# Kernel tuning notes

Measured on AMD Instinct MI355X. Metric: run time of the kernel, lower is better.

## Reference

```python
import jax, jax.numpy as jnp
import numpy as np

NUM_HEADS = 16
CHUNK = 64
RMS_EPS = 1.1920928955078125e-07  # torch.finfo(float32).eps, F.rms_norm default


def setup_inputs() -> dict:
    key = jax.random.key(0)
    k1, k2, k3 = jax.random.split(key, 3)
    B, S, D = 2, 4096, 2048
    x = jax.random.normal(k1, (B, S, D), dtype=jnp.float32)
    w_in = jax.random.normal(k2, (5 * D, D), dtype=jnp.float32) * 0.02
    w_out = jax.random.normal(k3, (D, D), dtype=jnp.float32) * 0.02
    return {"x": x, "w_in": w_in, "w_out": w_out}


def _forward(x, w_in, w_out):
    B, S, D = x.shape
    H, hd, C = NUM_HEADS, D // NUM_HEADS, CHUNK
    proj = x @ w_in.T                              # [B,S,5D]
    q, k, v, a, g = jnp.split(proj, 5, axis=-1)
    rs = lambda t: t.reshape(B, S, H, hd)
    q, k, v, a, g = map(rs, (q, k, v, a, g))
    # rms_norm over head_dim, no learned weight
    q = q * jax.lax.rsqrt(jnp.mean(q * q, axis=-1, keepdims=True) + RMS_EPS)
    k = jnp.tanh(k)
    a = jnp.clip(jax.nn.sigmoid(a + 2.0), 0.6, 0.9995)
    u = k * v                                      # updates, float32
    NC = S // C
    # [NC, B, C, H, hd] so lax.scan iterates over chunks
    a_r = a.reshape(B, NC, C, H, hd).transpose(1, 0, 2, 3, 4)
    u_r = u.reshape(B, NC, C, H, hd).transpose(1, 0, 2, 3, 4)

    def step(state, au):
        a_c, u_c = au                              # [B,C,H,hd]
        prefix = jnp.cumprod(a_c, axis=1)
        acc = jnp.cumsum(u_c / jnp.maximum(prefix, 1e-6), axis=1)
        states = prefix * (state[:, None] + acc)   # [B,C,H,hd]
        return states[:, -1], states

    state0 = jnp.zeros((B, H, hd), dtype=jnp.float32)
    _, mem = jax.lax.scan(step, state0, (a_r, u_r))  # [NC,B,C,H,hd]
    memory = mem.transpose(1, 0, 2, 3, 4).reshape(B, S, H, hd)
    gate = jax.nn.sigmoid(g)
    y = gate * (q * memory) + (1.0 - gate) * v
    return y.reshape(B, S, D) @ w_out.T


def reference(x, w_in, w_out):
    return _forward(x, w_in, w_out)
```

## Files before the change

### kernel.cpp

```cpp
#include <hip/hip_runtime.h>
#include <cstdint>
#include <cstddef>

typedef unsigned short u16;
typedef __bf16 bf16x8 __attribute__((ext_vector_type(8)));
typedef unsigned int u32;
typedef u32 u32x4 __attribute__((ext_vector_type(4)));
typedef float f32x4v __attribute__((ext_vector_type(4)));

#define BB 2
#define SS 4096
#define DD 2048
#define HH 16
#define HD 128
#define CC 64
#define NC 64
#define D5 10240
#define RMS_EPS 1.1920928955078125e-07f

__device__ __forceinline__ u16 f2bf(float f) {
  uint32_t x = __float_as_uint(f);
  uint32_t r = (x + 0x7fffu + ((x >> 16) & 1u)) >> 16;
  return (u16)r;
}
__device__ __forceinline__ float bf2f(u16 u) {
  return __uint_as_float(((uint32_t)u) << 16);
}
__device__ __forceinline__ float fast_sigmoid(float x) {
  return 1.0f / (1.0f + __expf(-x));
}
__device__ __forceinline__ float fast_tanh(float x) {
  return 1.0f - 2.0f / (__expf(2.0f * x) + 1.0f);
}

__global__ void cvt_bf16x8_kernel(const f32x4v* __restrict__ src,
                                  u32x4* __restrict__ dst, int n8) {
  int i = blockIdx.x * blockDim.x + threadIdx.x;
  int stride = gridDim.x * blockDim.x;
  for (; i < n8; i += stride) {
    f32x4v a = src[2 * i];
    f32x4v b = src[2 * i + 1];
    u32x4 o;
    o.x = (u32)f2bf(a.x) | ((u32)f2bf(a.y) << 16);
    o.y = (u32)f2bf(a.z) | ((u32)f2bf(a.w) << 16);
    o.z = (u32)f2bf(b.x) | ((u32)f2bf(b.y) << 16);
    o.w = (u32)f2bf(b.z) | ((u32)f2bf(b.w) << 16);
    dst[i] = o;
  }
}

template <typename OutT>
__global__ __launch_bounds__(512, 2) void gemm_bt(const u16* __restrict__ A,
                                                  const u16* __restrict__ B,
                                                  OutT* __restrict__ C,
                                                  int M, int N, int K) {
  __shared__ u16 lds[65536];

  const int tid = threadIdx.x;
  const int wave = tid >> 6;
  const int lane = tid & 63;

  const int nwg = (int)gridDim.x;
  const int bid = (int)blockIdx.x;
  const int bswz = (bid & 7) * (nwg >> 3) + (bid >> 3);
  const int Mt = M >> 8;
  const int m0 = (bswz % Mt) << 8;
  const int n0 = (bswz / Mt) << 8;

  const int wm = (wave >> 2) << 7;
  const int wn = (wave & 3) << 6;

  const int s_r = tid >> 3;
  const int s_ls = (tid & 7) ^ (s_r & 7);
  const u16* Ast = A + (size_t)(m0 + s_r) * K + s_ls * 8;
  const u16* Bst = B + (size_t)(n0 + s_r) * K + s_ls * 8;
  const int s_lb = wave * 512;

  const int fr = lane & 15;
  const int fg = lane >> 4;
  const int fx = lane & 7;
  const int psk0 = ((0 + fg) ^ fx) * 8;
  const int psk1 = ((4 + fg) ^ fx) * 8;
  const int aro = (wm + fr) * 64;
  const int bro = 16384 + (wn + fr) * 64;

  f32x4v acc[8][4] = {};
  bf16x8 afr[4][2];
  bf16x8 bfr[2][2][2];
  const int NT = K >> 6;

#define BARF()                              \
  do {                                      \
    asm volatile("" ::: "memory");          \
    __builtin_amdgcn_s_barrier();           \
    asm volatile("" ::: "memory");          \
  } while (0)

#define STAGE(GB, LB, H, KT)                                                    \
  do {                                                                          \
    const u16* g_ = (GB) + (size_t)((H) * 128) * K + (KT) * 64;                 \
    __builtin_amdgcn_global_load_lds(                                           \
        (__attribute__((address_space(1))) void*)(u16*)g_,                      \
        (__attribute__((address_space(3))) void*)&lds[(LB) + (H) * 8192 + s_lb],\
        16, 0, 0);                                                              \
    __builtin_amdgcn_global_load_lds(                                           \
        (__attribute__((address_space(1))) void*)(u16*)(g_ + (size_t)64 * K),   \
        (__attribute__((address_space(3))) void*)&lds[(LB) + (H) * 8192 + 4096 + s_lb], \
        16, 0, 0);                                                              \
  } while (0)

#define LOADA(BO, MH)                                             \
  do {                                                            \
    _Pragma("unroll") for (int mf = 0; mf < 4; ++mf) {            \
      const int ab_ = (BO) + aro + (MH) * 4096 + mf * 1024;       \
      afr[mf][0] = *(const bf16x8*)&lds[ab_ + psk0];              \
      afr[mf][1] = *(const bf16x8*)&lds[ab_ + psk1];              \
    }                                                             \
  } while (0)

#define LOADB(BO, NH)                                             \
  do {                                                            \
    _Pragma("unroll") for (int nf = 0; nf < 2; ++nf) {            \
      const int bb_ = (BO) + bro + (NH) * 2048 + nf * 1024;       \
      bfr[NH][nf][0] = *(const bf16x8*)&lds[bb_ + psk0];          \
      bfr[NH][nf][1] = *(const bf16x8*)&lds[bb_ + psk1];          \
    }                                                             \
  } while (0)

#define MMAQ(MH, NH)                                                          \
  do {                                                                        \
    __builtin_amdgcn_s_setprio(1);                                            \
    _Pragma("unroll") for (int mf = 0; mf < 4; ++mf)                          \
        _Pragma("unroll") for (int nf = 0; nf < 2; ++nf) {                    \
      acc[(MH) * 4 + mf][(NH) * 2 + nf] =                                     \
          __builtin_amdgcn_mfma_f32_16x16x32_bf16(                            \
              afr[mf][0], bfr[NH][nf][0], acc[(MH) * 4 + mf][(NH) * 2 + nf],  \
              0, 0, 0);                                                       \
      acc[(MH) * 4 + mf][(NH) * 2 + nf] =                                     \
          __builtin_amdgcn_mfma_f32_16x16x32_bf16(                            \
              afr[mf][1], bfr[NH][nf][1], acc[(MH) * 4 + mf][(NH) * 2 + nf],  \
              0, 0, 0);                                                       \
    }                                                                         \
    __builtin_amdgcn_s_setprio(0);                                            \
    __builtin_amdgcn_sched_barrier(0);                                        \
  } while (0)

  STAGE(Ast, 0, 0, 0);
  STAGE(Ast, 0, 1, 0);
  STAGE(Bst, 16384, 0, 0);
  STAGE(Bst, 16384, 1, 0);
  {
    const int k1 = (NT > 1) ? 1 : 0;
    STAGE(Ast, 32768, 0, k1);
    STAGE(Ast, 32768, 1, k1);
    STAGE(Bst, 49152, 0, k1);
    STAGE(Bst, 49152, 1, k1);
  }
  asm volatile("s_waitcnt vmcnt(8)" ::: "memory");
  BARF();

  for (int t = 0; t < NT; ++t) {
    const int bo = (t & 1) << 15;
    const int t2 = (t + 2 < NT) ? t + 2 : NT - 1;

    LOADA(bo, 0);
    LOADB(bo, 0);
    BARF();
    MMAQ(0, 0);
    BARF();

    LOADB(bo, 1);
    BARF();
    MMAQ(0, 1);
    BARF();

    LOADA(bo, 1);
    BARF();
    MMAQ(1, 1);
    BARF();

    STAGE(Ast, bo, 0, t2);
    STAGE(Bst, bo + 16384, 0, t2);
    STAGE(Ast, bo, 1, t2);
    STAGE(Bst, bo + 16384, 1, t2);
    BARF();
    MMAQ(1, 0);
    asm volatile("s_waitcnt vmcnt(8)" ::: "memory");
    BARF();
  }

  asm volatile("s_waitcnt vmcnt(0)" ::: "memory");

  const int ccol = lane & 15;
  const int crow = (lane >> 4) << 2;
#pragma unroll
  for (int am = 0; am < 8; ++am) {
    const size_t r0 = (size_t)(m0 + wm + ((am >> 2) << 6) + ((am & 3) << 4) + crow);
#pragma unroll
    for (int an = 0; an < 4; ++an) {
      const size_t c0 = (size_t)(n0 + wn + ((an >> 1) << 5) + ((an & 1) << 4) + ccol);
#pragma unroll
      for (int r = 0; r < 4; ++r) {
        OutT* Cp = C + (r0 + r) * (size_t)N + c0;
        if constexpr (sizeof(OutT) == 2)
          *Cp = (OutT)f2bf(acc[am][an][r]);
        else
          *Cp = acc[am][an][r];
      }
    }
  }
#undef BARF
#undef STAGE
#undef LOADA
#undef LOADB
#undef MMAQ
}

__global__ __launch_bounds__(64) void scan_chunk(const u16* __restrict__ proj,
                                                 float* __restrict__ Pc,
                                                 float* __restrict__ Lc) {
  const int idx = blockIdx.x;
  const int h = idx & (HH - 1);
  const int c = (idx >> 4) & (NC - 1);
  const int b = idx >> 10;
  const int lane = threadIdx.x;

  const size_t row0 = (size_t)(b * SS + c * CC) * D5 + h * HD;

  float p0 = 1.0f, a0 = 0.0f, p1 = 1.0f, a1 = 0.0f;
  for (int t = 0; t < CC; ++t) {
    const size_t rp = row0 + (size_t)t * D5;
    float k0 = bf2f(proj[rp + DD + lane]);
    float k1 = bf2f(proj[rp + DD + lane + 64]);
    float v0 = bf2f(proj[rp + 2 * DD + lane]);
    float v1 = bf2f(proj[rp + 2 * DD + lane + 64]);
    float ar0 = bf2f(proj[rp + 3 * DD + lane]);
    float ar1 = bf2f(proj[rp + 3 * DD + lane + 64]);
    float aa0 = fminf(fmaxf(fast_sigmoid(ar0 + 2.0f), 0.6f), 0.9995f);
    float aa1 = fminf(fmaxf(fast_sigmoid(ar1 + 2.0f), 0.6f), 0.9995f);
    p0 *= aa0;
    p1 *= aa1;
    a0 += fast_tanh(k0) * v0 / fmaxf(p0, 1e-6f);
    a1 += fast_tanh(k1) * v1 / fmaxf(p1, 1e-6f);
  }
  const size_t ci = ((size_t)(b * NC + c) * HH + h) * HD;
  Pc[ci + lane] = p0;
  Pc[ci + lane + 64] = p1;
  Lc[ci + lane] = p0 * a0;
  Lc[ci + lane + 64] = p1 * a1;
}

__global__ void scan_carry(const float* __restrict__ Pc, const float* __restrict__ Lc,
                           float* __restrict__ Sin) {
  const int t = blockIdx.x * blockDim.x + threadIdx.x;
  const int b = t >> 11;
  const int hd = t & (DD - 1);
  float state = 0.0f;
  for (int c = 0; c < NC; ++c) {
    const size_t i = (size_t)(b * NC + c) * DD + hd;
    Sin[i] = state;
    state = Pc[i] * state + Lc[i];
  }
}

__global__ __launch_bounds__(64) void finalize_y(const u16* __restrict__ proj,
                                                 const float* __restrict__ Sin,
                                                 u16* __restrict__ y) {
  const int idx = blockIdx.x;
  const int h = idx & (HH - 1);
  const int c = (idx >> 4) & (NC - 1);
  const int b = idx >> 10;
  const int lane = threadIdx.x;

  const size_t row0 = (size_t)(b * SS + c * CC) * D5 + h * HD;
  const size_t out0 = (size_t)(b * SS + c * CC) * DD + h * HD;
  const size_t sinb = (size_t)(b * NC + c) * DD + h * HD;
  const float sin0 = Sin[sinb + lane];
  const float sin1 = Sin[sinb + lane + 64];

  float p0 = 1.0f, a0 = 0.0f, p1 = 1.0f, a1 = 0.0f;
  for (int t = 0; t < CC; ++t) {
    const size_t rp = row0 + (size_t)t * D5;
    const float q0 = bf2f(proj[rp + lane]);
    const float q1 = bf2f(proj[rp + lane + 64]);
    const float k0 = bf2f(proj[rp + DD + lane]);
    const float k1 = bf2f(proj[rp + DD + lane + 64]);
    const float v0 = bf2f(proj[rp + 2 * DD + lane]);
    const float v1 = bf2f(proj[rp + 2 * DD + lane + 64]);
    const float ar0 = bf2f(proj[rp + 3 * DD + lane]);
    const float ar1 = bf2f(proj[rp + 3 * DD + lane + 64]);
    const float g0 = bf2f(proj[rp + 4 * DD + lane]);
    const float g1 = bf2f(proj[rp + 4 * DD + lane + 64]);

    const float aa0 = fminf(fmaxf(fast_sigmoid(ar0 + 2.0f), 0.6f), 0.9995f);
    const float aa1 = fminf(fmaxf(fast_sigmoid(ar1 + 2.0f), 0.6f), 0.9995f);
    p0 *= aa0;
    p1 *= aa1;
    a0 += fast_tanh(k0) * v0 / fmaxf(p0, 1e-6f);
    a1 += fast_tanh(k1) * v1 / fmaxf(p1, 1e-6f);
    const float mem0 = p0 * (sin0 + a0);
    const float mem1 = p1 * (sin1 + a1);

    float ss = q0 * q0 + q1 * q1;
#pragma unroll
    for (int m = 32; m; m >>= 1) ss += __shfl_xor(ss, m);
    const float rn = rsqrtf(ss * (1.0f / 128.0f) + RMS_EPS);

    const float gt0 = fast_sigmoid(g0);
    const float gt1 = fast_sigmoid(g1);
    y[out0 + (size_t)t * DD + lane] = f2bf(gt0 * (q0 * rn * mem0) + (1.0f - gt0) * v0);
    y[out0 + (size_t)t * DD + lane + 64] = f2bf(gt1 * (q1 * rn * mem1) + (1.0f - gt1) * v1);
  }
}

extern "C" void kernel_launch(void* const* d_in, const int* in_sizes, int n_in,
                              void* d_out, int out_size, void* d_ws, size_t ws_size,
                              hipStream_t stream) {
  const float* x = (const float*)d_in[0];
  const float* w_in = (const float*)d_in[1];
  const float* w_out = (const float*)d_in[2];
  float* out = (float*)d_out;

  char* ws = (char*)d_ws;
  size_t off = 0;
  auto alloc = [&](size_t bytes) -> void* {
    void* p = ws + off;
    off += (bytes + 255) & ~(size_t)255;
    return p;
  };
  const size_t nBS = (size_t)BB * SS;
  u16* projb = (u16*)alloc(nBS * D5 * 2);
  u16* xb    = (u16*)alloc(nBS * DD * 2);
  u16* wib   = (u16*)alloc((size_t)D5 * DD * 2);
  u16* wob   = (u16*)alloc((size_t)DD * DD * 2);
  float* Pc  = (float*)alloc((size_t)BB * NC * DD * 4);
  float* Lc  = (float*)alloc((size_t)BB * NC * DD * 4);
  float* Sin = (float*)alloc((size_t)BB * NC * DD * 4);
  u16* yb = xb;
  (void)in_sizes; (void)n_in; (void)out_size;

  if (off > ws_size) return;

  cvt_bf16x8_kernel<<<1024, 256, 0, stream>>>((const f32x4v*)x, (u32x4*)xb,
                                              (int)(nBS * DD / 8));
  cvt_bf16x8_kernel<<<1024, 256, 0, stream>>>((const f32x4v*)w_in, (u32x4*)wib,
                                              (int)((size_t)D5 * DD / 8));
  cvt_bf16x8_kernel<<<1024, 256, 0, stream>>>((const f32x4v*)w_out, (u32x4*)wob,
                                              (int)((size_t)DD * DD / 8));

  gemm_bt<u16><<<dim3(32 * 40), 512, 0, stream>>>(xb, wib, projb, 8192, 10240, 2048);

  scan_chunk<<<BB * NC * HH, 64, 0, stream>>>(projb, Pc, Lc);

  scan_carry<<<16, 256, 0, stream>>>(Pc, Lc, Sin);

  finalize_y<<<BB * NC * HH, 64, 0, stream>>>(projb, Sin, yb);

  gemm_bt<float><<<dim3(32 * 8), 512, 0, stream>>>(yb, wob, out, 8192, 2048, 2048);
}
```

Before: 690.7 us.

## Remove intra-iteration barriers in GEMM loop and stage bf16 epilogue through LDS

Drops most workgroup barriers and sched_barriers inside the GEMM main loop. LDS fragment loads are now issued ahead of the MFMA groups so the compiler can interleave them, cutting sync stalls per k-tile. For bf16 output, the epilogue writes accumulators into a swizzled per-wave LDS tile and then stores 16-byte vectors to global memory, replacing scattered 2-byte stores. Fewer barriers risk correctness if the LDS staging buffer is overwritten while other waves still read it, and prefetching more fragments raises register pressure.

```diff
diff --git a/kernel.cpp b/kernel.cpp
--- a/kernel.cpp
+++ b/kernel.cpp
@@ -142,7 +142,6 @@
               0, 0, 0);                                                       \
     }                                                                         \
     __builtin_amdgcn_s_setprio(0);                                            \
-    __builtin_amdgcn_sched_barrier(0);                                        \
   } while (0)
 
   STAGE(Ast, 0, 0, 0);
@@ -165,47 +164,63 @@
 
     LOADA(bo, 0);
     LOADB(bo, 0);
-    BARF();
+    LOADB(bo, 1);
     MMAQ(0, 0);
-    BARF();
-
-    LOADB(bo, 1);
-    BARF();
     MMAQ(0, 1);
-    BARF();
-
     LOADA(bo, 1);
-    BARF();
     MMAQ(1, 1);
+    __builtin_amdgcn_sched_barrier(0);
     BARF();
 
     STAGE(Ast, bo, 0, t2);
     STAGE(Bst, bo + 16384, 0, t2);
     STAGE(Ast, bo, 1, t2);
     STAGE(Bst, bo + 16384, 1, t2);
-    BARF();
     MMAQ(1, 0);
     asm volatile("s_waitcnt vmcnt(8)" ::: "memory");
     BARF();
   }
 
   asm volatile("s_waitcnt vmcnt(0)" ::: "memory");
+  BARF();
 
   const int ccol = lane & 15;
   const int crow = (lane >> 4) << 2;
-#pragma unroll
-  for (int am = 0; am < 8; ++am) {
-    const size_t r0 = (size_t)(m0 + wm + ((am >> 2) << 6) + ((am & 3) << 4) + crow);
-#pragma unroll
-    for (int an = 0; an < 4; ++an) {
-      const size_t c0 = (size_t)(n0 + wn + ((an >> 1) << 5) + ((an & 1) << 4) + ccol);
-#pragma unroll
-      for (int r = 0; r < 4; ++r) {
-        OutT* Cp = C + (r0 + r) * (size_t)N + c0;
-        if constexpr (sizeof(OutT) == 2)
-          *Cp = (OutT)f2bf(acc[am][an][r]);
-        else
+  if constexpr (sizeof(OutT) == 2) {
+    u16* wlds = &lds[wave * 8192];
+#pragma unroll
+    for (int am = 0; am < 8; ++am) {
+#pragma unroll
+      for (int an = 0; an < 4; ++an) {
+        const int col = ((an >> 1) << 5) + ((an & 1) << 4) + ccol;
+        const int cch = col >> 3, cre = col & 7;
+#pragma unroll
+        for (int r = 0; r < 4; ++r) {
+          const int row = ((am >> 2) << 6) + ((am & 3) << 4) + crow + r;
+          wlds[row * 64 + ((cch ^ (row & 7)) << 3) + cre] =
+              f2bf(acc[am][an][r]);
+        }
+      }
+    }
+#pragma unroll
+    for (int i = 0; i < 16; ++i) {
+      const int row = i * 8 + (lane >> 3);
+      const int ch = lane & 7;
+      const u32x4 vv = *(const u32x4*)&wlds[row * 64 + (((ch) ^ (row & 7)) << 3)];
+      *(u32x4*)(C + (size_t)(m0 + wm + row) * N + (n0 + wn + ch * 8)) = vv;
+    }
+  } else {
+#pragma unroll
+    for (int am = 0; am < 8; ++am) {
+      const size_t r0 = (size_t)(m0 + wm + ((am >> 2) << 6) + ((am & 3) << 4) + crow);
+#pragma unroll
+      for (int an = 0; an < 4; ++an) {
+        const size_t c0 = (size_t)(n0 + wn + ((an >> 1) << 5) + ((an & 1) << 4) + ccol);
+#pragma unroll
+        for (int r = 0; r < 4; ++r) {
+          OutT* Cp = C + (r0 + r) * (size_t)N + c0;
           *Cp = acc[am][an][r];
+        }
       }
     }
   }
```

After: 657.5 us. -4.8%, faster.
